# Optimization experiments

Measured on AMD Instinct MI355X. Metric: run time of the kernel, lower is better.

The kernel has to match this reference:

```python
import jax, jax.numpy as jnp
import numpy as np

# Hyperparameters from module __init__
U_TH = 1.0      # firing threshold
BETA = 0.5      # membrane decay
BATCH_SIZE = 128
DELTA = 0.05    # ZO smoothing radius


def setup_inputs() -> dict:
    key = jax.random.key(0)
    k1, k2 = jax.random.split(key)
    T, B, F = 32, BATCH_SIZE, 8192
    inputs = jax.random.normal(k1, (T * B, F), dtype=jnp.float32)
    # 'sample once' Gaussian ZO tangents, same shape as inputs
    random_tangents = jax.random.normal(k2, (T * B, F), dtype=jnp.float32)
    return {"inputs": inputs, "random_tangents": random_tangents}


def reference(inputs, random_tangents):
    """Leaky integrate-and-fire over time with LocalZO (single-sample)
    surrogate gradient. inputs: [T*B, F] with T = leading//BATCH_SIZE."""
    orig_shape = inputs.shape
    T = inputs.shape[0] // BATCH_SIZE
    x = inputs.reshape(T, BATCH_SIZE, *inputs.shape[1:])
    z = random_tangents.reshape(T, BATCH_SIZE, *inputs.shape[1:])

    def step(u, xt_zt):
        xt, zt = xt_zt
        u = BETA * u + xt                      # membrane update
        v = u - U_TH                           # distance to threshold
        # LocalZO single-sample surrogate: |z|/(2*delta) * 1(|v| < delta*|z|)
        surr = jax.lax.stop_gradient(
            (jnp.abs(zt) / (2.0 * DELTA))
            * (jnp.abs(v) < DELTA * jnp.abs(zt)).astype(xt.dtype)
        )
        h = (v > 0).astype(xt.dtype)           # hard spike
        # straight-through: forward = h, d spike / d v = surr
        spike = jax.lax.stop_gradient(h - surr * v) + surr * v
        u = u - spike * U_TH                   # soft reset (subtract threshold)
        return u, spike

    u0 = jnp.zeros_like(x[0])
    _, spikes = jax.lax.scan(step, u0, (x, z))
    return spikes.reshape(orig_shape)
```

## Files before the change

### kernel.cpp

```cpp
#include <hip/hip_runtime.h>


constexpr int BATCH = 128;
constexpr int FDIM  = 8192;
constexpr int STEP  = BATCH * FDIM;
constexpr int VEC   = 4;
constexpr int PF    = 8;

typedef float v4f __attribute__((ext_vector_type(4)));

__device__ __forceinline__ void lif_step(const v4f xt, const v4f zt,
                                         v4f& u, v4f& ss)
{
#pragma clang fp contract(off)
#pragma unroll
    for (int c = 0; c < VEC; ++c) {
        float uu = 0.5f * u[c];
        uu = uu + xt[c];
        float v = uu - 1.0f;
        float az   = fabsf(zt[c]);
        float thr  = 0.05f * az;
        float ind  = (fabsf(v) < thr) ? 1.0f : 0.0f;
        float surr = (az / 0.1f) * ind;
        float h = (v > 0.0f) ? 1.0f : 0.0f;
        float a     = surr * v;
        float spike = (h - a) + a;
        u[c]  = uu - spike * 1.0f;
        ss[c] = spike;
    }
}

template<int T>
__global__ __launch_bounds__(256, 4) void lif_zo_unrolled(
    const float* __restrict__ x,
    const float* __restrict__ z,
    float* __restrict__ out)
{
#pragma clang fp contract(off)
    const int tid = blockIdx.x * blockDim.x + threadIdx.x;
    const long base = (long)tid * VEC;

    v4f u = {0.0f, 0.0f, 0.0f, 0.0f};

    v4f xb[PF], zb[PF];
#pragma unroll
    for (int j = 0; j < PF; ++j) {
        xb[j] = *reinterpret_cast<const v4f*>(x + base + (long)j * STEP);
        zb[j] = *reinterpret_cast<const v4f*>(z + base + (long)j * STEP);
    }

#pragma unroll
    for (int t = 0; t < T; ++t) {
        const int c = t % PF;
        const v4f xt = xb[c];
        const v4f zt = zb[c];
        if (t + PF < T) {
            xb[c] = *reinterpret_cast<const v4f*>(x + base + (long)(t + PF) * STEP);
            zb[c] = *reinterpret_cast<const v4f*>(z + base + (long)(t + PF) * STEP);
        }
        v4f ss;
        lif_step(xt, zt, u, ss);
        *reinterpret_cast<v4f*>(out + base + (long)t * STEP) = ss;
    }
}

__global__ __launch_bounds__(256, 4) void lif_zo_generic(
    const float* __restrict__ x,
    const float* __restrict__ z,
    float* __restrict__ out,
    int T)
{
#pragma clang fp contract(off)
    const int tid = blockIdx.x * blockDim.x + threadIdx.x;
    long idx = (long)tid * VEC;
    v4f u = {0.0f, 0.0f, 0.0f, 0.0f};
    for (int t = 0; t < T; ++t, idx += STEP) {
        const v4f xt = *reinterpret_cast<const v4f*>(x + idx);
        const v4f zt = *reinterpret_cast<const v4f*>(z + idx);
        v4f ss;
        lif_step(xt, zt, u, ss);
        *reinterpret_cast<v4f*>(out + idx) = ss;
    }
}

extern "C" void kernel_launch(void* const* d_in, const int* in_sizes, int n_in,
                              void* d_out, int out_size, void* d_ws, size_t ws_size,
                              hipStream_t stream)
{
    const float* x = (const float*)d_in[0];
    const float* z = (const float*)d_in[1];
    float* out = (float*)d_out;

    const int total = in_sizes[0];
    const int T = total / STEP;

    const int nthreads = STEP / VEC;
    const int block = 256;
    const int grid = nthreads / block;

    if (T == 32) {
        lif_zo_unrolled<32><<<grid, block, 0, stream>>>(x, z, out);
    } else {
        lif_zo_generic<<<grid, block, 0, stream>>>(x, z, out, T);
    }
}
```

Before: 313.1 us.

## Stream inputs through LDS with async global_load_lds multi-stage pipeline

Result: no change. 310.4 us (-0.8%).

```diff
diff --git a/kernel.cpp b/kernel.cpp
--- a/kernel.cpp
+++ b/kernel.cpp
@@ -5,9 +5,15 @@
 constexpr int FDIM  = 8192;
 constexpr int STEP  = BATCH * FDIM;
 constexpr int VEC   = 4;
-constexpr int PF    = 8;
+constexpr int D     = 4;
+constexpr int A     = 3;
 
 typedef float v4f __attribute__((ext_vector_type(4)));
+
+#define GLD16(gsrc, ldst)                                                  \
+    __builtin_amdgcn_global_load_lds(                                      \
+        (const __attribute__((address_space(1))) unsigned int*)(gsrc),     \
+        (__attribute__((address_space(3))) unsigned int*)(ldst), 16, 0, 0)
 
 __device__ __forceinline__ void lif_step(const v4f xt, const v4f zt,
                                          v4f& u, v4f& ss)
@@ -30,41 +36,54 @@
     }
 }
 
-template<int T>
-__global__ __launch_bounds__(256, 4) void lif_zo_unrolled(
+__global__ __launch_bounds__(256) void lif_zo_lds(
     const float* __restrict__ x,
     const float* __restrict__ z,
-    float* __restrict__ out)
+    float* __restrict__ out,
+    int T)
 {
 #pragma clang fp contract(off)
-    const int tid = blockIdx.x * blockDim.x + threadIdx.x;
-    const long base = (long)tid * VEC;
+    __shared__ v4f buf[D][2][256];
+
+    const int  ltid  = threadIdx.x;
+    const int  gtid  = blockIdx.x * 256 + ltid;
+    const long base  = (long)gtid * VEC;
+    const int  wbase = ltid & ~63;
+
+    auto stage = [&](int s) {
+        const int slot = s & (D - 1);
+        GLD16(x + base + (long)s * STEP, &buf[slot][0][wbase]);
+        GLD16(z + base + (long)s * STEP, &buf[slot][1][wbase]);
+    };
+
+#pragma unroll
+    for (int j = 0; j < A; ++j) stage(j);
 
     v4f u = {0.0f, 0.0f, 0.0f, 0.0f};
 
-    v4f xb[PF], zb[PF];
-#pragma unroll
-    for (int j = 0; j < PF; ++j) {
-        xb[j] = *reinterpret_cast<const v4f*>(x + base + (long)j * STEP);
-        zb[j] = *reinterpret_cast<const v4f*>(z + base + (long)j * STEP);
-    }
+    for (int t = 0; t < T; ++t) {
+        const int slot = t & (D - 1);
+        if (t < A) {
+            asm volatile("s_waitcnt vmcnt(4)" ::: "memory");
+        } else if (t < T - A + 1) {
+            asm volatile("s_waitcnt vmcnt(6)" ::: "memory");
+        } else {
+            asm volatile("s_waitcnt vmcnt(2)" ::: "memory");
+        }
+        __builtin_amdgcn_sched_barrier(0);
 
-#pragma unroll
-    for (int t = 0; t < T; ++t) {
-        const int c = t % PF;
-        const v4f xt = xb[c];
-        const v4f zt = zb[c];
-        if (t + PF < T) {
-            xb[c] = *reinterpret_cast<const v4f*>(x + base + (long)(t + PF) * STEP);
-            zb[c] = *reinterpret_cast<const v4f*>(z + base + (long)(t + PF) * STEP);
-        }
+        const v4f xt = buf[slot][0][ltid];
+        const v4f zt = buf[slot][1][ltid];
+
         v4f ss;
         lif_step(xt, zt, u, ss);
         *reinterpret_cast<v4f*>(out + base + (long)t * STEP) = ss;
+
+        if (t + A < T) stage(t + A);
     }
 }
 
-__global__ __launch_bounds__(256, 4) void lif_zo_generic(
+__global__ __launch_bounds__(256) void lif_zo_generic(
     const float* __restrict__ x,
     const float* __restrict__ z,
     float* __restrict__ out,
@@ -98,8 +117,8 @@
     const int block = 256;
     const int grid = nthreads / block;
 
-    if (T == 32) {
-        lif_zo_unrolled<32><<<grid, block, 0, stream>>>(x, z, out);
+    if (T >= 2 * A) {
+        lif_zo_lds<<<grid, block, 0, stream>>>(x, z, out, T);
     } else {
         lif_zo_generic<<<grid, block, 0, stream>>>(x, z, out, T);
     }
```
